# Kernel optimization log

Hardware: AMD Instinct MI355X
Metric: run time of the kernel (lower is better)

The kernel has to match this reference:

```python
import jax, jax.numpy as jnp
import numpy as np

KH = KW = 3
SH = SW = 1
PAD = 1
IN_LEN = 8
OUT_LEN = 16
NUM_ITERS = 3


def squash(t, axis=-1):
    sq = jnp.sum(t * t, axis=axis, keepdims=True)
    return (sq / (1.0 + sq)) * t / jnp.sqrt(sq)


def setup_inputs() -> dict:
    key = jax.random.key(0)
    k1, k2 = jax.random.split(key)
    x = jax.random.normal(k1, (4, 64, 32, 32), dtype=jnp.float32)
    # weight: (out_channels//out_length, C_in//in_length * kh*kw, out_length, in_length)
    weight = jax.random.normal(k2, (8, 72, 16, 8), dtype=jnp.float32)
    return {"x": x, "weight": weight}


def reference(x, weight):
    N, C, H, W = x.shape
    O = weight.shape[0]
    L = OUT_LEN
    G = C // IN_LEN  # number of input capsule groups
    Ho = 1 + (H + 2 * PAD - KH) // SH
    Wo = 1 + (W + 2 * PAD - KW) // SW

    # im2col: (N, C*KH*KW, Ho, Wo), feature dim ordered channel-major, kernel-spatial-minor
    patches = jax.lax.conv_general_dilated_patches(
        x, (KH, KW), (SH, SW), [(PAD, PAD), (PAD, PAD)])
    # -> (N, G, in_length, kk, Ho*Wo)
    pt = patches.reshape(N, G, IN_LEN, KH * KW, Ho * Wo)
    # -> (N, HW, G, kk, in_length), matching torch's unfold/view/transpose chain
    pt = jnp.transpose(pt, (0, 4, 1, 3, 2))
    win = pt.reshape(N, Ho * Wo, G * KH * KW, IN_LEN)

    priors = jnp.einsum('oflp,nwfp->nowfl', weight, win)
    priors = priors.reshape(N, O, Ho * Wo, G, KH * KW, L)

    # dynamic routing
    probs = jnp.ones(priors.shape[:-1] + (1,), priors.dtype)
    outputs = None
    for r in range(NUM_ITERS):
        s = jnp.mean(jnp.sum(probs * priors, axis=-2, keepdims=True),
                     axis=-3, keepdims=True)  # (N,O,HW,1,1,L)
        outputs = squash(s)
        if r != NUM_ITERS - 1:
            delta = jnp.sum(priors * outputs, axis=-1, keepdims=True)
            probs = probs + jnp.exp(delta)

    out = outputs[:, :, :, 0, 0, :]                    # (N, O, HW, L)
    out = jnp.transpose(out, (0, 1, 3, 2))             # (N, O, L, HW)
    return out.reshape(N, O * L, Ho, Wo)
```

## Files before the change

kernel.cpp:

```cpp
#include <hip/hip_runtime.h>
#include <hip/hip_bf16.h>


typedef short bf16x8 __attribute__((ext_vector_type(8)));
typedef float f32x4 __attribute__((ext_vector_type(4)));

__global__ void prep_w(const float* __restrict__ w, ushort* __restrict__ wT) {
  const int t = blockIdx.x * 256 + threadIdx.x;
  if (t >= 9216) return;
  const float* src = w + t * 8;
  uint hi[4], lo[4];
  #pragma unroll
  for (int p2 = 0; p2 < 4; ++p2) {
    float v0 = src[p2 * 2], v1 = src[p2 * 2 + 1];
    __hip_bfloat16 h0 = __float2bfloat16(v0);
    __hip_bfloat16 h1 = __float2bfloat16(v1);
    __hip_bfloat16 l0 = __float2bfloat16(v0 - __bfloat162float(h0));
    __hip_bfloat16 l1 = __float2bfloat16(v1 - __bfloat162float(h1));
    hi[p2] = (uint)(*(ushort*)&h0) | ((uint)(*(ushort*)&h1) << 16);
    lo[p2] = (uint)(*(ushort*)&l0) | ((uint)(*(ushort*)&l1) << 16);
  }
  uint* dst = (uint*)(wT + t * 16);
  *(uint4*)dst       = make_uint4(hi[0], hi[1], hi[2], hi[3]);
  *(uint4*)(dst + 4) = make_uint4(lo[0], lo[1], lo[2], lo[3]);
}

__global__ void prep_x(const float* __restrict__ x, ushort* __restrict__ xT) {
  const int t = blockIdx.x * 256 + threadIdx.x;
  const int pix = t >> 3, oct = t & 7;
  const int n = pix >> 10, hw = pix & 1023;
  const float* src = x + n * 65536 + oct * 8 * 1024 + hw;
  ushort* dst = xT + pix * 128 + oct * 8;
  #pragma unroll
  for (int k = 0; k < 8; ++k) {
    float v = src[k * 1024];
    __hip_bfloat16 h = __float2bfloat16(v);
    __hip_bfloat16 l = __float2bfloat16(v - __bfloat162float(h));
    dst[k]      = *(ushort*)&h;
    dst[64 + k] = *(ushort*)&l;
  }
}

__global__ __launch_bounds__(256, 4)
void caps_main(const ushort* __restrict__ wT, const ushort* __restrict__ xT,
               float* __restrict__ out) {
  const int b  = blockIdx.x;
  const int wt = b & 1, h = (b >> 1) & 31, o = (b >> 6) & 7, n = b >> 9;
  const int w0 = wt * 16;
  const int tid = threadIdx.x, lane = tid & 63, fq = tid >> 6;
  const int pix = lane & 15, q = lane >> 4;

  __shared__ uint  xs[54 * 68];
  __shared__ float sbuf[4 * 16 * 16];

  for (int i = tid; i < 54 * 16; i += 256) {
    const int r = i >> 4, seg = i & 15;
    const int kh = r / 18, c = r % 18;
    const int hh = h + kh - 1, ww = w0 + c - 1;
    uint4 v = make_uint4(0u, 0u, 0u, 0u);
    if ((unsigned)hh < 32u && (unsigned)ww < 32u) {
      const uint* g = (const uint*)xT + (n * 1024 + hh * 32 + ww) * 64 + seg * 4;
      v = *(const uint4*)g;
    }
    *(uint4*)&xs[r * 68 + seg * 4] = v;
  }
  __syncthreads();

  f32x4 P[18];
  const f32x4 zacc = {0.f, 0.f, 0.f, 0.f};
  const ushort* wA = wT + ((o * 72 + fq * 18) * 16 + pix) * 16 + ((q == 2) ? 8 : 0);
  const bool aload = (q < 3);
  const int xw_lane = pix * 68 + ((q == 1) ? 32 : 0);
  #pragma unroll
  for (int j = 0; j < 18; ++j) {
    const int g = fq * 2 + (j >= 9 ? 1 : 0);
    const int s = j % 9, kh = s / 3, kw = s % 3;
    bf16x8 a = {0, 0, 0, 0, 0, 0, 0, 0};
    if (aload) a = *(const bf16x8*)(wA + j * 256);
    const bf16x8 bv = *(const bf16x8*)&xs[(kh * 18 + kw) * 68 + g * 4 + xw_lane];
    P[j] = __builtin_amdgcn_mfma_f32_16x16x32_bf16(a, bv, zacc, 0, 0, 0);
  }

  float c[18];
  #pragma unroll
  for (int j = 0; j < 18; ++j) c[j] = 1.f;

  const int sidx = pix * 16 + (q << 2);
  #pragma unroll
  for (int it = 0; it < 3; ++it) {
    f32x4 sp = {0.f, 0.f, 0.f, 0.f};
    #pragma unroll
    for (int j = 0; j < 18; ++j) {
      sp.x += c[j] * P[j].x; sp.y += c[j] * P[j].y;
      sp.z += c[j] * P[j].z; sp.w += c[j] * P[j].w;
    }
    if (it) __syncthreads();
    *(f32x4*)&sbuf[fq * 256 + sidx] = sp;
    __syncthreads();
    f32x4 S0 = *(const f32x4*)&sbuf[0 * 256 + sidx];
    f32x4 S1 = *(const f32x4*)&sbuf[1 * 256 + sidx];
    f32x4 S2 = *(const f32x4*)&sbuf[2 * 256 + sidx];
    f32x4 S3 = *(const f32x4*)&sbuf[3 * 256 + sidx];
    f32x4 sv;
    sv.x = (S0.x + S1.x + S2.x + S3.x) * 0.125f;
    sv.y = (S0.y + S1.y + S2.y + S3.y) * 0.125f;
    sv.z = (S0.z + S1.z + S2.z + S3.z) * 0.125f;
    sv.w = (S0.w + S1.w + S2.w + S3.w) * 0.125f;
    float qq = sv.x * sv.x + sv.y * sv.y + sv.z * sv.z + sv.w * sv.w;
    qq += __shfl_xor(qq, 16);
    qq += __shfl_xor(qq, 32);
    const float k = sqrtf(qq) / (1.f + qq);
    f32x4 ov;
    ov.x = sv.x * k; ov.y = sv.y * k; ov.z = sv.z * k; ov.w = sv.w * k;
    if (it < 2) {
      #pragma unroll
      for (int j = 0; j < 18; ++j) {
        float d = P[j].x * ov.x + P[j].y * ov.y + P[j].z * ov.z + P[j].w * ov.w;
        d += __shfl_xor(d, 16);
        d += __shfl_xor(d, 32);
        c[j] += __expf(d);
      }
    } else if (fq == 0) {
      float* op = out + ((n * 8 + o) * 16 + (q << 2)) * 1024 + h * 32 + w0 + pix;
      op[0]    = ov.x;
      op[1024] = ov.y;
      op[2048] = ov.z;
      op[3072] = ov.w;
    }
  }
}

extern "C" void kernel_launch(void* const* d_in, const int* in_sizes, int n_in,
                              void* d_out, int out_size, void* d_ws, size_t ws_size,
                              hipStream_t stream) {
  const float* x = (const float*)d_in[0];
  const float* w = (const float*)d_in[1];
  float* outp    = (float*)d_out;
  ushort* wT = (ushort*)d_ws;
  ushort* xT = (ushort*)((char*)d_ws + 294912);
  prep_w<<<dim3(36), dim3(256), 0, stream>>>(w, wT);
  prep_x<<<dim3(128), dim3(256), 0, stream>>>(x, xT);
  caps_main<<<dim3(2048), dim3(256), 0, stream>>>(wT, xT, outp);
}
```

Measured before the change: 82.09 us.

## Merge prep kernels, transpose x via LDS, and double-buffer routing reduction buffer

Folds the weight and input preprocessing into one launch, which removes a kernel launch. The input half now stages each tile through LDS so that global reads and writes are both coalesced, instead of strided 2-byte stores. The main kernel double-buffers the cross-wave reduction buffer to drop one barrier per routing iteration. It also lets the fourth lane group do a lo*lo MFMA instead of masking its loads, and relaxes the occupancy hint from 4 to 3 blocks per CU, which could change register allocation.

```diff
diff --git a/kernel.cpp b/kernel.cpp
--- a/kernel.cpp
+++ b/kernel.cpp
@@ -5,43 +5,63 @@
 typedef short bf16x8 __attribute__((ext_vector_type(8)));
 typedef float f32x4 __attribute__((ext_vector_type(4)));
 
-__global__ void prep_w(const float* __restrict__ w, ushort* __restrict__ wT) {
-  const int t = blockIdx.x * 256 + threadIdx.x;
-  if (t >= 9216) return;
-  const float* src = w + t * 8;
-  uint hi[4], lo[4];
-  #pragma unroll
-  for (int p2 = 0; p2 < 4; ++p2) {
-    float v0 = src[p2 * 2], v1 = src[p2 * 2 + 1];
-    __hip_bfloat16 h0 = __float2bfloat16(v0);
-    __hip_bfloat16 h1 = __float2bfloat16(v1);
-    __hip_bfloat16 l0 = __float2bfloat16(v0 - __bfloat162float(h0));
-    __hip_bfloat16 l1 = __float2bfloat16(v1 - __bfloat162float(h1));
-    hi[p2] = (uint)(*(ushort*)&h0) | ((uint)(*(ushort*)&h1) << 16);
-    lo[p2] = (uint)(*(ushort*)&l0) | ((uint)(*(ushort*)&l1) << 16);
-  }
-  uint* dst = (uint*)(wT + t * 16);
-  *(uint4*)dst       = make_uint4(hi[0], hi[1], hi[2], hi[3]);
-  *(uint4*)(dst + 4) = make_uint4(lo[0], lo[1], lo[2], lo[3]);
+__device__ __forceinline__ uint pack_split(float v) {
+  __hip_bfloat16 hb = __float2bfloat16(v);
+  float hf = __bfloat162float(hb);
+  __hip_bfloat16 lb = __float2bfloat16(v - hf);
+  return (uint)(*(ushort*)&hb) | ((uint)(*(ushort*)&lb) << 16);
 }
 
-__global__ void prep_x(const float* __restrict__ x, ushort* __restrict__ xT) {
-  const int t = blockIdx.x * 256 + threadIdx.x;
-  const int pix = t >> 3, oct = t & 7;
-  const int n = pix >> 10, hw = pix & 1023;
-  const float* src = x + n * 65536 + oct * 8 * 1024 + hw;
-  ushort* dst = xT + pix * 128 + oct * 8;
-  #pragma unroll
-  for (int k = 0; k < 8; ++k) {
-    float v = src[k * 1024];
-    __hip_bfloat16 h = __float2bfloat16(v);
-    __hip_bfloat16 l = __float2bfloat16(v - __bfloat162float(h));
-    dst[k]      = *(ushort*)&h;
-    dst[64 + k] = *(ushort*)&l;
+__global__ __launch_bounds__(256)
+void prep(const float* __restrict__ x, const float* __restrict__ w,
+          ushort* __restrict__ wT, ushort* __restrict__ xT) {
+  const int b = blockIdx.x;
+  if (b < 32) {
+    __shared__ uint lds[128 * 65];
+    const int n = b >> 3, h0 = (b & 7) * 4;
+    const float* src = x + n * 65536 + h0 * 32;
+    for (int i = threadIdx.x; i < 8192; i += 256) {
+      const int c = i >> 7, p = i & 127;
+      lds[p * 65 + c] = pack_split(src[c * 1024 + p]);
+    }
+    __syncthreads();
+    uint* dst = (uint*)xT + (n * 1024 + h0 * 32) * 64;
+    for (int i = threadIdx.x; i < 2048; i += 256) {
+      const int pix = i >> 4, seg = i & 15;
+      const uint* row = &lds[pix * 65 + (seg & 7) * 8];
+      uint4 v;
+      if (seg < 8) {
+        v.x = (row[0] & 0xffffu) | (row[1] << 16);
+        v.y = (row[2] & 0xffffu) | (row[3] << 16);
+        v.z = (row[4] & 0xffffu) | (row[5] << 16);
+        v.w = (row[6] & 0xffffu) | (row[7] << 16);
+      } else {
+        v.x = (row[0] >> 16) | (row[1] & 0xffff0000u);
+        v.y = (row[2] >> 16) | (row[3] & 0xffff0000u);
+        v.z = (row[4] >> 16) | (row[5] & 0xffff0000u);
+        v.w = (row[6] >> 16) | (row[7] & 0xffff0000u);
+      }
+      *(uint4*)(dst + pix * 64 + seg * 4) = v;
+    }
+  } else {
+    const int t = (b - 32) * 256 + threadIdx.x;
+    if (t >= 9216) return;
+    const float* src = w + t * 8;
+    uint hi[4], lo[4];
+    #pragma unroll
+    for (int p2 = 0; p2 < 4; ++p2) {
+      uint a = pack_split(src[p2 * 2]);
+      uint c = pack_split(src[p2 * 2 + 1]);
+      hi[p2] = (a & 0xffffu) | (c << 16);
+      lo[p2] = (a >> 16) | (c & 0xffff0000u);
+    }
+    uint* dstp = (uint*)(wT + t * 16);
+    *(uint4*)dstp       = make_uint4(hi[0], hi[1], hi[2], hi[3]);
+    *(uint4*)(dstp + 4) = make_uint4(lo[0], lo[1], lo[2], lo[3]);
   }
 }
 
-__global__ __launch_bounds__(256, 4)
+__global__ __launch_bounds__(256, 3)
 void caps_main(const ushort* __restrict__ wT, const ushort* __restrict__ xT,
                float* __restrict__ out) {
   const int b  = blockIdx.x;
@@ -51,7 +71,7 @@
   const int pix = lane & 15, q = lane >> 4;
 
   __shared__ uint  xs[54 * 68];
-  __shared__ float sbuf[4 * 16 * 16];
+  __shared__ float sbuf[2][4 * 256];
 
   for (int i = tid; i < 54 * 16; i += 256) {
     const int r = i >> 4, seg = i & 15;
@@ -68,15 +88,13 @@
 
   f32x4 P[18];
   const f32x4 zacc = {0.f, 0.f, 0.f, 0.f};
-  const ushort* wA = wT + ((o * 72 + fq * 18) * 16 + pix) * 16 + ((q == 2) ? 8 : 0);
-  const bool aload = (q < 3);
-  const int xw_lane = pix * 68 + ((q == 1) ? 32 : 0);
+  const ushort* wA = wT + ((o * 72 + fq * 18) * 16 + pix) * 16 + ((q >= 2) ? 8 : 0);
+  const int xw_lane = pix * 68 + ((q & 1) ? 32 : 0);
   #pragma unroll
   for (int j = 0; j < 18; ++j) {
     const int g = fq * 2 + (j >= 9 ? 1 : 0);
     const int s = j % 9, kh = s / 3, kw = s % 3;
-    bf16x8 a = {0, 0, 0, 0, 0, 0, 0, 0};
-    if (aload) a = *(const bf16x8*)(wA + j * 256);
+    const bf16x8 a  = *(const bf16x8*)(wA + j * 256);
     const bf16x8 bv = *(const bf16x8*)&xs[(kh * 18 + kw) * 68 + g * 4 + xw_lane];
     P[j] = __builtin_amdgcn_mfma_f32_16x16x32_bf16(a, bv, zacc, 0, 0, 0);
   }
@@ -94,18 +112,16 @@
       sp.x += c[j] * P[j].x; sp.y += c[j] * P[j].y;
       sp.z += c[j] * P[j].z; sp.w += c[j] * P[j].w;
     }
-    if (it) __syncthreads();
-    *(f32x4*)&sbuf[fq * 256 + sidx] = sp;
+    float* sb = sbuf[it & 1];
+    *(f32x4*)&sb[fq * 256 + sidx] = sp;
     __syncthreads();
-    f32x4 S0 = *(const f32x4*)&sbuf[0 * 256 + sidx];
-    f32x4 S1 = *(const f32x4*)&sbuf[1 * 256 + sidx];
-    f32x4 S2 = *(const f32x4*)&sbuf[2 * 256 + sidx];
-    f32x4 S3 = *(const f32x4*)&sbuf[3 * 256 + sidx];
-    f32x4 sv;
-    sv.x = (S0.x + S1.x + S2.x + S3.x) * 0.125f;
-    sv.y = (S0.y + S1.y + S2.y + S3.y) * 0.125f;
-    sv.z = (S0.z + S1.z + S2.z + S3.z) * 0.125f;
-    sv.w = (S0.w + S1.w + S2.w + S3.w) * 0.125f;
+    f32x4 sv = *(const f32x4*)&sb[sidx];
+    #pragma unroll
+    for (int k4 = 1; k4 < 4; ++k4) {
+      f32x4 t = *(const f32x4*)&sb[k4 * 256 + sidx];
+      sv.x += t.x; sv.y += t.y; sv.z += t.z; sv.w += t.w;
+    }
+    sv.x *= 0.125f; sv.y *= 0.125f; sv.z *= 0.125f; sv.w *= 0.125f;
     float qq = sv.x * sv.x + sv.y * sv.y + sv.z * sv.z + sv.w * sv.w;
     qq += __shfl_xor(qq, 16);
     qq += __shfl_xor(qq, 32);
@@ -138,7 +154,6 @@
   float* outp    = (float*)d_out;
   ushort* wT = (ushort*)d_ws;
   ushort* xT = (ushort*)((char*)d_ws + 294912);
-  prep_w<<<dim3(36), dim3(256), 0, stream>>>(w, wT);
-  prep_x<<<dim3(128), dim3(256), 0, stream>>>(x, xT);
+  prep<<<dim3(68), dim3(256), 0, stream>>>(x, w, wT, xT);
   caps_main<<<dim3(2048), dim3(256), 0, stream>>>(wT, xT, outp);
 }
```

Measured after the change: 78.16 us. 4.8% less time.
